# Performance work log

Hardware: AMD Instinct MI355X
Metric: run time of the kernel (lower is better)

## Reference

```python
import jax, jax.numpy as jnp
import numpy as np

EMB = 1024
HEADS = 16
BLOCK = 128


def setup_inputs() -> dict:
    key = jax.random.key(0)
    k1, k2, k3 = jax.random.split(key, 3)
    B, T, C = 4, 4096, EMB
    x = jax.random.normal(k1, (B, T, C), dtype=jnp.float32)
    # Linear weights stored as [in, out] (i.e. torch W.T); qkv has no bias.
    W_qkv = jax.random.normal(k2, (C, 3 * C), dtype=jnp.float32) * 0.02
    W_proj = jax.random.normal(k3, (C, C), dtype=jnp.float32) * 0.02
    b_proj = jnp.zeros((C,), dtype=jnp.float32)
    return {"x": x, "W_qkv": W_qkv, "W_proj": W_proj, "b_proj": b_proj}


def reference(x, W_qkv, W_proj, b_proj):
    # Dropout is inference-mode identity.
    B, T, C = x.shape
    H, D, BS = HEADS, C // HEADS, BLOCK
    nb = T // BS  # number of local blocks
    qkv = x @ W_qkv  # [B,T,3C]
    q, k, v = jnp.split(qkv, 3, axis=-1)
    # [B, nb, BS, H, D] -- each block attends only within itself
    q = q.reshape(B, nb, BS, H, D)
    k = k.reshape(B, nb, BS, H, D)
    v = v.reshape(B, nb, BS, H, D)
    scores = jnp.einsum("bnqhd,bnkhd->bnhqk", q, k) / jnp.sqrt(jnp.float32(D))
    # is_decoder: causal tril within each diagonal block (tril[i:end, i:end])
    tril = jnp.tril(jnp.ones((BS, BS), dtype=bool))
    scores = jnp.where(tril, scores, -jnp.inf)
    # faithful to original: stable exp, then divide by (sum + 1e-6)
    scores = scores - jnp.max(scores, axis=-1, keepdims=True)
    e = jnp.exp(scores)
    p = e / (jnp.sum(e, axis=-1, keepdims=True) + 1e-6)
    out = jnp.einsum("bnhqk,bnkhd->bnqhd", p, v).reshape(B, T, C)
    return out @ W_proj + b_proj
```

## Files before the change

kernel.cpp:

```cpp
#include <hip/hip_runtime.h>
#include <hip/hip_bf16.h>
#include <math.h>


typedef __bf16 bf16_t;
typedef __bf16 bf16x8 __attribute__((ext_vector_type(8)));
typedef float  f32x4  __attribute__((ext_vector_type(4)));

typedef const __attribute__((address_space(1))) void* gptr_t;
typedef __attribute__((address_space(3))) void* lptr_t;

__global__ __launch_bounds__(256) void cvt_f32_bf16(const float* __restrict__ in,
                                                    bf16_t* __restrict__ out, size_t n) {
    size_t stride = (size_t)gridDim.x * blockDim.x * 4;
    for (size_t i = ((size_t)blockIdx.x * blockDim.x + threadIdx.x) * 4; i < n; i += stride) {
        float4 v = *(const float4*)(in + i);
        bf16_t t[4];
        t[0] = (bf16_t)v.x; t[1] = (bf16_t)v.y; t[2] = (bf16_t)v.z; t[3] = (bf16_t)v.w;
        *(uint2*)(out + i) = *(uint2*)t;
    }
}

__global__ __launch_bounds__(256) void transpose_cvt(const float* __restrict__ in,
                                                     bf16_t* __restrict__ out, int K, int N) {
    __shared__ float tile[32][33];
    const int tx = threadIdx.x & 31, ty = threadIdx.x >> 5;
    const int bx = blockIdx.x, by = blockIdx.y;
    #pragma unroll
    for (int i = 0; i < 4; i++) {
        const int k = by * 32 + ty + i * 8;
        tile[ty + i * 8][tx] = in[(size_t)k * N + bx * 32 + tx];
    }
    __syncthreads();
    #pragma unroll
    for (int i = 0; i < 4; i++) {
        const int n = bx * 32 + ty + i * 8;
        out[(size_t)n * K + by * 32 + tx] = (bf16_t)tile[tx][ty + i * 8];
    }
}

template <bool BF16_OUT, bool BIAS>
__global__ __launch_bounds__(256) void gemm_bt(const bf16_t* __restrict__ A,
                                               const bf16_t* __restrict__ Bt,
                                               void* __restrict__ Cout,
                                               const float* __restrict__ bias,
                                               int M, int N, int K) {
    __shared__ bf16_t As[2][128 * 32];
    __shared__ bf16_t Bs[2][128 * 32];

    const int bn = blockIdx.x, bm = blockIdx.y;
    const int tid = threadIdx.x;
    const int lane = tid & 63, wave = tid >> 6;
    const int wm = wave >> 1, wn = wave & 1;
    const int quad = lane >> 4, l16 = lane & 15;

    const bf16_t* Ab = A  + (size_t)bm * 128 * K;
    const bf16_t* Bb = Bt + (size_t)bn * 128 * K;

    f32x4 acc[4][4];
    for (int i = 0; i < 4; i++)
        for (int j = 0; j < 4; j++)
            acc[i][j] = (f32x4){0.f, 0.f, 0.f, 0.f};

    const int srow = lane >> 2;
    const int scb  = (lane & 3) * 16;

    for (int k0 = 0; k0 < K; k0 += 64) {
        #pragma unroll
        for (int half = 0; half < 2; half++) {
            #pragma unroll
            for (int i = 0; i < 2; i++) {
                const int s = wave * 2 + i;
                const int row = s * 16 + srow;
                const int kk = k0 + half * 32;
                __builtin_amdgcn_global_load_lds(
                    (gptr_t)((const char*)(Ab + (size_t)row * K + kk) + scb),
                    (lptr_t)&As[half][s * 512], 16, 0, 0);
                __builtin_amdgcn_global_load_lds(
                    (gptr_t)((const char*)(Bb + (size_t)row * K + kk) + scb),
                    (lptr_t)&Bs[half][s * 512], 16, 0, 0);
            }
        }
        __syncthreads();

        #pragma unroll
        for (int half = 0; half < 2; half++) {
            bf16x8 af[4], bf[4];
            #pragma unroll
            for (int mr = 0; mr < 4; mr++)
                af[mr] = *(const bf16x8*)&As[half][(wm * 64 + mr * 16 + l16) * 32 + quad * 8];
            #pragma unroll
            for (int nr = 0; nr < 4; nr++)
                bf[nr] = *(const bf16x8*)&Bs[half][(wn * 64 + nr * 16 + l16) * 32 + quad * 8];
            #pragma unroll
            for (int mr = 0; mr < 4; mr++)
                #pragma unroll
                for (int nr = 0; nr < 4; nr++)
                    acc[mr][nr] = __builtin_amdgcn_mfma_f32_16x16x32_bf16(af[mr], bf[nr], acc[mr][nr], 0, 0, 0);
        }
        __syncthreads();
    }

    #pragma unroll
    for (int mr = 0; mr < 4; mr++) {
        #pragma unroll
        for (int nr = 0; nr < 4; nr++) {
            const int gcol = bn * 128 + wn * 64 + nr * 16 + l16;
            #pragma unroll
            for (int reg = 0; reg < 4; reg++) {
                const int grow = bm * 128 + wm * 64 + mr * 16 + quad * 4 + reg;
                float v = acc[mr][nr][reg];
                if (BIAS) v += bias[gcol];
                if (BF16_OUT)
                    ((bf16_t*)Cout)[(size_t)grow * N + gcol] = (bf16_t)v;
                else
                    ((float*)Cout)[(size_t)grow * N + gcol] = v;
            }
        }
    }
}

__global__ __launch_bounds__(256, 3) void attn_kernel(const bf16_t* __restrict__ qkv,
                                                      bf16_t* __restrict__ attn_out) {
    __shared__ __align__(16) char smem[54272];
    bf16_t* qs = (bf16_t*)smem;
    bf16_t* ks = (bf16_t*)(smem + 18432);
    bf16_t* vT = (bf16_t*)(smem + 36864);
    bf16_t* ps = (bf16_t*)smem;

    const int tid = threadIdx.x;
    const int lane = tid & 63, wave = tid >> 6;
    const int quad = lane >> 4, l16 = lane & 15;

    const int bid = blockIdx.x;
    const int h = bid & 15;
    const int blk = (bid >> 4) & 31;
    const int b = bid >> 9;
    const int row0 = (b * 32 + blk) * 128;
    const int LDQ = 3072;

    const int wu = __builtin_amdgcn_readfirstlane(wave);
    const int g0 = wu, g1 = 7 - wu;

    for (int t = tid; t < 128 * 8; t += 256) {
        const int r = t >> 3;
        const int c = (t & 7) * 8;
        const bf16_t* src = qkv + (size_t)(row0 + r) * LDQ + h * 64;
        *(uint4*)&qs[r * 72 + c] = *(const uint4*)(src + c);
        *(uint4*)&ks[r * 72 + c] = *(const uint4*)(src + 1024 + c);
        bf16x8 vv = *(const bf16x8*)(src + 2048 + c);
        #pragma unroll
        for (int j = 0; j < 8; j++)
            vT[(c + j) * 136 + r] = vv[j];
    }
    __syncthreads();

    f32x4 sfrag[2][8];
    for (int mr = 0; mr < 2; mr++)
        for (int nc = 0; nc < 8; nc++)
            sfrag[mr][nc] = (f32x4){0.f, 0.f, 0.f, 0.f};

    #pragma unroll
    for (int ksl = 0; ksl < 2; ksl++) {
        bf16x8 aq0 = *(const bf16x8*)&qs[(g0 * 16 + l16) * 72 + ksl * 32 + quad * 8];
        bf16x8 aq1 = *(const bf16x8*)&qs[(g1 * 16 + l16) * 72 + ksl * 32 + quad * 8];
        #pragma unroll
        for (int nc = 0; nc < 8; nc++) {
            if (nc <= g1) {
                bf16x8 bk = *(const bf16x8*)&ks[(nc * 16 + l16) * 72 + ksl * 32 + quad * 8];
                sfrag[1][nc] = __builtin_amdgcn_mfma_f32_16x16x32_bf16(aq1, bk, sfrag[1][nc], 0, 0, 0);
                if (nc <= g0)
                    sfrag[0][nc] = __builtin_amdgcn_mfma_f32_16x16x32_bf16(aq0, bk, sfrag[0][nc], 0, 0, 0);
            }
        }
    }

    #pragma unroll
    for (int mr = 0; mr < 2; mr++) {
        const int g = mr ? g1 : g0;
        #pragma unroll
        for (int nc = 0; nc < 8; nc++) {
            #pragma unroll
            for (int reg = 0; reg < 4; reg++) {
                const int row = g * 16 + quad * 4 + reg;
                const int col = nc * 16 + l16;
                float s = sfrag[mr][nc][reg] * 0.125f;
                if (col > row) s = -INFINITY;
                sfrag[mr][nc][reg] = s;
            }
        }
    }

    #pragma unroll
    for (int mr = 0; mr < 2; mr++) {
        #pragma unroll
        for (int reg = 0; reg < 4; reg++) {
            float m = -INFINITY;
            #pragma unroll
            for (int nc = 0; nc < 8; nc++) m = fmaxf(m, sfrag[mr][nc][reg]);
            #pragma unroll
            for (int off = 1; off < 16; off <<= 1) m = fmaxf(m, __shfl_xor(m, off));
            float sum = 0.f;
            #pragma unroll
            for (int nc = 0; nc < 8; nc++) {
                float e = __expf(sfrag[mr][nc][reg] - m);
                sfrag[mr][nc][reg] = e;
                sum += e;
            }
            #pragma unroll
            for (int off = 1; off < 16; off <<= 1) sum += __shfl_xor(sum, off);
            const float inv = 1.0f / (sum + 1e-6f);
            #pragma unroll
            for (int nc = 0; nc < 8; nc++) sfrag[mr][nc][reg] *= inv;
        }
    }

    __syncthreads();

    #pragma unroll
    for (int mr = 0; mr < 2; mr++) {
        const int g = mr ? g1 : g0;
        const int rbase = g * 16 + quad * 4;
        #pragma unroll
        for (int nc = 0; nc < 8; nc++)
            #pragma unroll
            for (int reg = 0; reg < 4; reg++)
                ps[(rbase + reg) * 136 + nc * 16 + l16] = (bf16_t)sfrag[mr][nc][reg];
    }
    __syncthreads();

    f32x4 oacc[2][4];
    for (int mr = 0; mr < 2; mr++)
        for (int nd = 0; nd < 4; nd++)
            oacc[mr][nd] = (f32x4){0.f, 0.f, 0.f, 0.f};

    const int s0 = g0 >> 1, s1 = g1 >> 1;
    #pragma unroll
    for (int ksl = 0; ksl < 4; ksl++) {
        if (ksl <= s1) {
            bf16x8 ap1 = *(const bf16x8*)&ps[(g1 * 16 + l16) * 136 + ksl * 32 + quad * 8];
            bf16x8 ap0;
            const bool use0 = (ksl <= s0);
            if (use0)
                ap0 = *(const bf16x8*)&ps[(g0 * 16 + l16) * 136 + ksl * 32 + quad * 8];
            #pragma unroll
            for (int nd = 0; nd < 4; nd++) {
                bf16x8 bv = *(const bf16x8*)&vT[(nd * 16 + l16) * 136 + ksl * 32 + quad * 8];
                oacc[1][nd] = __builtin_amdgcn_mfma_f32_16x16x32_bf16(ap1, bv, oacc[1][nd], 0, 0, 0);
                if (use0)
                    oacc[0][nd] = __builtin_amdgcn_mfma_f32_16x16x32_bf16(ap0, bv, oacc[0][nd], 0, 0, 0);
            }
        }
    }

    #pragma unroll
    for (int mr = 0; mr < 2; mr++) {
        const int g = mr ? g1 : g0;
        #pragma unroll
        for (int nd = 0; nd < 4; nd++) {
            #pragma unroll
            for (int reg = 0; reg < 4; reg++) {
                const int row = row0 + g * 16 + quad * 4 + reg;
                const int col = h * 64 + nd * 16 + l16;
                attn_out[(size_t)row * 1024 + col] = (bf16_t)oacc[mr][nd][reg];
            }
        }
    }
}

extern "C" void kernel_launch(void* const* d_in, const int* in_sizes, int n_in,
                              void* d_out, int out_size, void* d_ws, size_t ws_size,
                              hipStream_t stream) {
    const float* x     = (const float*)d_in[0];
    const float* Wqkv  = (const float*)d_in[1];
    const float* Wproj = (const float*)d_in[2];
    const float* bproj = (const float*)d_in[3];

    const int M = 16384, C = 1024, N1 = 3072;

    char* ws = (char*)d_ws;
    bf16_t* xb     = (bf16_t*)(ws);
    bf16_t* wqkvT  = (bf16_t*)(ws + 33554432);
    bf16_t* wprojT = (bf16_t*)(ws + 39845888);
    bf16_t* qkvb   = (bf16_t*)(ws + 41943040);
    bf16_t* attnb  = (bf16_t*)(ws + 142606336);

    cvt_f32_bf16<<<8192, 256, 0, stream>>>(x, xb, (size_t)M * C);
    transpose_cvt<<<dim3(N1 / 32, C / 32), 256, 0, stream>>>(Wqkv, wqkvT, C, N1);
    transpose_cvt<<<dim3(C / 32, C / 32), 256, 0, stream>>>(Wproj, wprojT, C, C);

    gemm_bt<true, false><<<dim3(N1 / 128, M / 128), 256, 0, stream>>>(
        xb, wqkvT, (void*)qkvb, nullptr, M, N1, C);

    attn_kernel<<<2048, 256, 0, stream>>>(qkvb, attnb);

    gemm_bt<false, true><<<dim3(C / 128, M / 128), 256, 0, stream>>>(
        attnb, wprojT, d_out, bproj, M, C, C);
}
```

Before: 354.2 us.

## Fuse QKV projection GEMM into local attention kernel per head-block tile

Replaces the separate QKV GEMM and attention kernels with one kernel. Each 512-thread block computes the 128x192 Q/K/V tile for one head and one 128-row block directly into shared memory, then runs masked softmax attention on it. This removes the round trip of the 96MB bf16 qkv intermediate through global memory and one launch. In exchange, the GEMM tile is narrower (192 columns) with single-buffered global_load_lds staging and no overlap between loads and MFMA, which may lower GEMM efficiency.

Result: slower. 424.6 us (+19.9%).

```diff
diff --git a/kernel.cpp b/kernel.cpp
--- a/kernel.cpp
+++ b/kernel.cpp
@@ -120,150 +120,185 @@
     }
 }
 
-__global__ __launch_bounds__(256, 3) void attn_kernel(const bf16_t* __restrict__ qkv,
+__global__ __launch_bounds__(512) void fused_qkv_attn(const bf16_t* __restrict__ A,
+                                                      const bf16_t* __restrict__ Bt,
                                                       bf16_t* __restrict__ attn_out) {
     __shared__ __align__(16) char smem[54272];
-    bf16_t* qs = (bf16_t*)smem;
-    bf16_t* ks = (bf16_t*)(smem + 18432);
-    bf16_t* vT = (bf16_t*)(smem + 36864);
-    bf16_t* ps = (bf16_t*)smem;
+    bf16_t* As0 = (bf16_t*)smem;
+    bf16_t* Bs0 = (bf16_t*)(smem + 16384);
+    bf16_t* qs  = (bf16_t*)smem;
+    bf16_t* ks  = (bf16_t*)(smem + 18432);
+    bf16_t* vT  = (bf16_t*)(smem + 36864);
+    bf16_t* ps  = (bf16_t*)smem;
 
     const int tid = threadIdx.x;
     const int lane = tid & 63, wave = tid >> 6;
     const int quad = lane >> 4, l16 = lane & 15;
-
-    const int bid = blockIdx.x;
-    const int h = bid & 15;
-    const int blk = (bid >> 4) & 31;
-    const int b = bid >> 9;
-    const int row0 = (b * 32 + blk) * 128;
-    const int LDQ = 3072;
-
     const int wu = __builtin_amdgcn_readfirstlane(wave);
-    const int g0 = wu, g1 = 7 - wu;
-
-    for (int t = tid; t < 128 * 8; t += 256) {
-        const int r = t >> 3;
-        const int c = (t & 7) * 8;
-        const bf16_t* src = qkv + (size_t)(row0 + r) * LDQ + h * 64;
-        *(uint4*)&qs[r * 72 + c] = *(const uint4*)(src + c);
-        *(uint4*)&ks[r * 72 + c] = *(const uint4*)(src + 1024 + c);
-        bf16x8 vv = *(const bf16x8*)(src + 2048 + c);
-        #pragma unroll
-        for (int j = 0; j < 8; j++)
-            vT[(c + j) * 136 + r] = vv[j];
+    const int wm = wu >> 2, wn = wu & 3;
+
+    const int h  = blockIdx.x;
+    const int bm = blockIdx.y;
+    const int row0 = bm * 128;
+    const int K = 1024;
+
+    const bf16_t* Ab = A + (size_t)row0 * K;
+
+    f32x4 acc[4][3];
+    for (int i = 0; i < 4; i++)
+        for (int j = 0; j < 3; j++)
+            acc[i][j] = (f32x4){0.f, 0.f, 0.f, 0.f};
+
+    const int srow = lane >> 2;
+    const int scb  = (lane & 3) * 16;
+
+    for (int k0 = 0; k0 < K; k0 += 64) {
+        #pragma unroll
+        for (int half = 0; half < 2; half++) {
+            const int kk = k0 + half * 32;
+            {
+                const int row = wu * 16 + srow;
+                __builtin_amdgcn_global_load_lds(
+                    (gptr_t)((const char*)(Ab + (size_t)row * K + kk) + scb),
+                    (lptr_t)&As0[half * 4096 + wu * 512], 16, 0, 0);
+            }
+            {
+                const int s = wu;
+                const int grow = (s >> 2) * 1024 + h * 64 + (s & 3) * 16 + srow;
+                __builtin_amdgcn_global_load_lds(
+                    (gptr_t)((const char*)(Bt + (size_t)grow * K + kk) + scb),
+                    (lptr_t)&Bs0[half * 6144 + s * 512], 16, 0, 0);
+            }
+            if (wu < 4) {
+                const int s = 8 + wu;
+                const int grow = 2 * 1024 + h * 64 + (s & 3) * 16 + srow;
+                __builtin_amdgcn_global_load_lds(
+                    (gptr_t)((const char*)(Bt + (size_t)grow * K + kk) + scb),
+                    (lptr_t)&Bs0[half * 6144 + s * 512], 16, 0, 0);
+            }
+        }
+        __syncthreads();
+
+        #pragma unroll
+        for (int half = 0; half < 2; half++) {
+            bf16x8 af[4], bf[3];
+            #pragma unroll
+            for (int mr = 0; mr < 4; mr++)
+                af[mr] = *(const bf16x8*)&As0[half * 4096 + (wm * 64 + mr * 16 + l16) * 32 + quad * 8];
+            #pragma unroll
+            for (int nr = 0; nr < 3; nr++)
+                bf[nr] = *(const bf16x8*)&Bs0[half * 6144 + (wn * 48 + nr * 16 + l16) * 32 + quad * 8];
+            #pragma unroll
+            for (int mr = 0; mr < 4; mr++)
+                #pragma unroll
+                for (int nr = 0; nr < 3; nr++)
+                    acc[mr][nr] = __builtin_amdgcn_mfma_f32_16x16x32_bf16(af[mr], bf[nr], acc[mr][nr], 0, 0, 0);
+        }
+        __syncthreads();
+    }
+
+    #pragma unroll
+    for (int mr = 0; mr < 4; mr++) {
+        #pragma unroll
+        for (int nr = 0; nr < 3; nr++) {
+            const int gcol = wn * 48 + nr * 16 + l16;
+            #pragma unroll
+            for (int reg = 0; reg < 4; reg++) {
+                const int grow = wm * 64 + mr * 16 + quad * 4 + reg;
+                const bf16_t v = (bf16_t)acc[mr][nr][reg];
+                if (gcol < 64)       qs[grow * 72 + gcol] = v;
+                else if (gcol < 128) ks[grow * 72 + (gcol - 64)] = v;
+                else                 vT[(gcol - 128) * 136 + grow] = v;
+            }
+        }
     }
     __syncthreads();
 
-    f32x4 sfrag[2][8];
-    for (int mr = 0; mr < 2; mr++)
+    const int g = wu;
+
+    f32x4 sfrag[8];
+    for (int nc = 0; nc < 8; nc++) sfrag[nc] = (f32x4){0.f, 0.f, 0.f, 0.f};
+
+    #pragma unroll
+    for (int ksl = 0; ksl < 2; ksl++) {
+        bf16x8 aq = *(const bf16x8*)&qs[(g * 16 + l16) * 72 + ksl * 32 + quad * 8];
+        #pragma unroll
+        for (int nc = 0; nc < 8; nc++) {
+            if (nc <= g) {
+                bf16x8 bk = *(const bf16x8*)&ks[(nc * 16 + l16) * 72 + ksl * 32 + quad * 8];
+                sfrag[nc] = __builtin_amdgcn_mfma_f32_16x16x32_bf16(aq, bk, sfrag[nc], 0, 0, 0);
+            }
+        }
+    }
+
+    #pragma unroll
+    for (int nc = 0; nc < 8; nc++) {
+        #pragma unroll
+        for (int reg = 0; reg < 4; reg++) {
+            const int row = g * 16 + quad * 4 + reg;
+            const int col = nc * 16 + l16;
+            float s = sfrag[nc][reg] * 0.125f;
+            if (col > row) s = -INFINITY;
+            sfrag[nc][reg] = s;
+        }
+    }
+
+    #pragma unroll
+    for (int reg = 0; reg < 4; reg++) {
+        float m = -INFINITY;
+        #pragma unroll
+        for (int nc = 0; nc < 8; nc++) m = fmaxf(m, sfrag[nc][reg]);
+        #pragma unroll
+        for (int off = 1; off < 16; off <<= 1) m = fmaxf(m, __shfl_xor(m, off));
+        float sum = 0.f;
+        #pragma unroll
+        for (int nc = 0; nc < 8; nc++) {
+            float e = __expf(sfrag[nc][reg] - m);
+            sfrag[nc][reg] = e;
+            sum += e;
+        }
+        #pragma unroll
+        for (int off = 1; off < 16; off <<= 1) sum += __shfl_xor(sum, off);
+        const float inv = 1.0f / (sum + 1e-6f);
+        #pragma unroll
+        for (int nc = 0; nc < 8; nc++) sfrag[nc][reg] *= inv;
+    }
+
+    __syncthreads();
+
+    {
+        const int rbase = g * 16 + quad * 4;
+        #pragma unroll
         for (int nc = 0; nc < 8; nc++)
-            sfrag[mr][nc] = (f32x4){0.f, 0.f, 0.f, 0.f};
-
-    #pragma unroll
-    for (int ksl = 0; ksl < 2; ksl++) {
-        bf16x8 aq0 = *(const bf16x8*)&qs[(g0 * 16 + l16) * 72 + ksl * 32 + quad * 8];
-        bf16x8 aq1 = *(const bf16x8*)&qs[(g1 * 16 + l16) * 72 + ksl * 32 + quad * 8];
-        #pragma unroll
-        for (int nc = 0; nc < 8; nc++) {
-            if (nc <= g1) {
-                bf16x8 bk = *(const bf16x8*)&ks[(nc * 16 + l16) * 72 + ksl * 32 + quad * 8];
-                sfrag[1][nc] = __builtin_amdgcn_mfma_f32_16x16x32_bf16(aq1, bk, sfrag[1][nc], 0, 0, 0);
-                if (nc <= g0)
-                    sfrag[0][nc] = __builtin_amdgcn_mfma_f32_16x16x32_bf16(aq0, bk, sfrag[0][nc], 0, 0, 0);
-            }
-        }
-    }
-
-    #pragma unroll
-    for (int mr = 0; mr < 2; mr++) {
-        const int g = mr ? g1 : g0;
-        #pragma unroll
-        for (int nc = 0; nc < 8; nc++) {
-            #pragma unroll
-            for (int reg = 0; reg < 4; reg++) {
-                const int row = g * 16 + quad * 4 + reg;
-                const int col = nc * 16 + l16;
-                float s = sfrag[mr][nc][reg] * 0.125f;
-                if (col > row) s = -INFINITY;
-                sfrag[mr][nc][reg] = s;
-            }
-        }
-    }
-
-    #pragma unroll
-    for (int mr = 0; mr < 2; mr++) {
-        #pragma unroll
-        for (int reg = 0; reg < 4; reg++) {
-            float m = -INFINITY;
-            #pragma unroll
-            for (int nc = 0; nc < 8; nc++) m = fmaxf(m, sfrag[mr][nc][reg]);
-            #pragma unroll
-            for (int off = 1; off < 16; off <<= 1) m = fmaxf(m, __shfl_xor(m, off));
-            float sum = 0.f;
-            #pragma unroll
-            for (int nc = 0; nc < 8; nc++) {
-                float e = __expf(sfrag[mr][nc][reg] - m);
-                sfrag[mr][nc][reg] = e;
-                sum += e;
-            }
-            #pragma unroll
-            for (int off = 1; off < 16; off <<= 1) sum += __shfl_xor(sum, off);
-            const float inv = 1.0f / (sum + 1e-6f);
-            #pragma unroll
-            for (int nc = 0; nc < 8; nc++) sfrag[mr][nc][reg] *= inv;
-        }
-    }
-
+            #pragma unroll
+            for (int reg = 0; reg < 4; reg++)
+                ps[(rbase + reg) * 136 + nc * 16 + l16] = (bf16_t)sfrag[nc][reg];
+    }
     __syncthreads();
 
-    #pragma unroll
-    for (int mr = 0; mr < 2; mr++) {
-        const int g = mr ? g1 : g0;
-        const int rbase = g * 16 + quad * 4;
-        #pragma unroll
-        for (int nc = 0; nc < 8; nc++)
-            #pragma unroll
-            for (int reg = 0; reg < 4; reg++)
-                ps[(rbase + reg) * 136 + nc * 16 + l16] = (bf16_t)sfrag[mr][nc][reg];
-    }
-    __syncthreads();
-
-    f32x4 oacc[2][4];
-    for (int mr = 0; mr < 2; mr++)
-        for (int nd = 0; nd < 4; nd++)
-            oacc[mr][nd] = (f32x4){0.f, 0.f, 0.f, 0.f};
-
-    const int s0 = g0 >> 1, s1 = g1 >> 1;
+    f32x4 oacc[4];
+    for (int nd = 0; nd < 4; nd++) oacc[nd] = (f32x4){0.f, 0.f, 0.f, 0.f};
+
+    const int smax = g >> 1;
     #pragma unroll
     for (int ksl = 0; ksl < 4; ksl++) {
-        if (ksl <= s1) {
-            bf16x8 ap1 = *(const bf16x8*)&ps[(g1 * 16 + l16) * 136 + ksl * 32 + quad * 8];
-            bf16x8 ap0;
-            const bool use0 = (ksl <= s0);
-            if (use0)
-                ap0 = *(const bf16x8*)&ps[(g0 * 16 + l16) * 136 + ksl * 32 + quad * 8];
+        if (ksl <= smax) {
+            bf16x8 ap = *(const bf16x8*)&ps[(g * 16 + l16) * 136 + ksl * 32 + quad * 8];
             #pragma unroll
             for (int nd = 0; nd < 4; nd++) {
                 bf16x8 bv = *(const bf16x8*)&vT[(nd * 16 + l16) * 136 + ksl * 32 + quad * 8];
-                oacc[1][nd] = __builtin_amdgcn_mfma_f32_16x16x32_bf16(ap1, bv, oacc[1][nd], 0, 0, 0);
-                if (use0)
-                    oacc[0][nd] = __builtin_amdgcn_mfma_f32_16x16x32_bf16(ap0, bv, oacc[0][nd], 0, 0, 0);
-            }
-        }
-    }
-
-    #pragma unroll
-    for (int mr = 0; mr < 2; mr++) {
-        const int g = mr ? g1 : g0;
-        #pragma unroll
-        for (int nd = 0; nd < 4; nd++) {
-            #pragma unroll
-            for (int reg = 0; reg < 4; reg++) {
-                const int row = row0 + g * 16 + quad * 4 + reg;
-                const int col = h * 64 + nd * 16 + l16;
-                attn_out[(size_t)row * 1024 + col] = (bf16_t)oacc[mr][nd][reg];
-            }
+                oacc[nd] = __builtin_amdgcn_mfma_f32_16x16x32_bf16(ap, bv, oacc[nd], 0, 0, 0);
+            }
+        }
+    }
+
+    #pragma unroll
+    for (int nd = 0; nd < 4; nd++) {
+        #pragma unroll
+        for (int reg = 0; reg < 4; reg++) {
+            const int row = row0 + g * 16 + quad * 4 + reg;
+            const int col = h * 64 + nd * 16 + l16;
+            attn_out[(size_t)row * 1024 + col] = (bf16_t)oacc[nd][reg];
         }
     }
 }
@@ -282,17 +317,13 @@
     bf16_t* xb     = (bf16_t*)(ws);
     bf16_t* wqkvT  = (bf16_t*)(ws + 33554432);
     bf16_t* wprojT = (bf16_t*)(ws + 39845888);
-    bf16_t* qkvb   = (bf16_t*)(ws + 41943040);
-    bf16_t* attnb  = (bf16_t*)(ws + 142606336);
+    bf16_t* attnb  = (bf16_t*)(ws + 41943040);
 
     cvt_f32_bf16<<<8192, 256, 0, stream>>>(x, xb, (size_t)M * C);
     transpose_cvt<<<dim3(N1 / 32, C / 32), 256, 0, stream>>>(Wqkv, wqkvT, C, N1);
     transpose_cvt<<<dim3(C / 32, C / 32), 256, 0, stream>>>(Wproj, wprojT, C, C);
 
-    gemm_bt<true, false><<<dim3(N1 / 128, M / 128), 256, 0, stream>>>(
-        xb, wqkvT, (void*)qkvb, nullptr, M, N1, C);
-
-    attn_kernel<<<2048, 256, 0, stream>>>(qkvb, attnb);
+    fused_qkv_attn<<<dim3(16, 128), 512, 0, stream>>>(xb, wqkvT, attnb);
 
     gemm_bt<false, true><<<dim3(C / 128, M / 128), 256, 0, stream>>>(
         attnb, wprojT, d_out, bproj, M, C, C);
```
